# Kernel tuning notes

Hardware: AMD Instinct MI355X
Metric: run time of the kernel (lower is better)

Reference implementation:

```python
import jax, jax.numpy as jnp
import numpy as np

N, E, G = 100000, 800000, 1000
N_IN, NHID, HEADS, NOUT = 128, 32, 4, 768
HC = NHID * HEADS


def setup_inputs() -> dict:
    key = jax.random.key(0)
    ks = jax.random.split(key, 12)
    s = 1.0 / np.sqrt(N_IN)
    inp = {
        "x": jax.random.normal(ks[0], (N, N_IN), jnp.float32),
        "edge_index": jax.random.randint(ks[1], (2, E), 0, N, jnp.int64),
        "batch": jnp.sort(jax.random.randint(ks[2], (N,), 0, G, jnp.int64)),
        "Wq": jax.random.uniform(ks[3], (N_IN, HC), jnp.float32, -s, s),
        "bq": jnp.zeros((HC,), jnp.float32),
        "Wk": jax.random.uniform(ks[4], (N_IN, HC), jnp.float32, -s, s),
        "bk": jnp.zeros((HC,), jnp.float32),
        "Wv": jax.random.uniform(ks[5], (N_IN, HC), jnp.float32, -s, s),
        "bv": jnp.zeros((HC,), jnp.float32),
        "Wskip": jax.random.uniform(ks[6], (N_IN, HC), jnp.float32, -s, s),
        "bskip": jnp.zeros((HC,), jnp.float32),
        "Wbeta": jax.random.uniform(ks[7], (3 * HC, 1), jnp.float32, -1.0 / np.sqrt(3 * HC), 1.0 / np.sqrt(3 * HC)),
        "W2": jax.random.uniform(ks[8], (HC, NOUT), jnp.float32, -1.0 / np.sqrt(HC), 1.0 / np.sqrt(HC)),
        "b2": jnp.zeros((NOUT,), jnp.float32),
    }
    return inp


def _transformer_net(x, edge_index, batch, Wq, bq, Wk, bk, Wv, bv, Wskip, bskip, Wbeta, W2, b2):
    src, dst = edge_index[0], edge_index[1]  # messages src -> dst
    q = (x @ Wq + bq).reshape(N, HEADS, NHID)
    k = (x @ Wk + bk).reshape(N, HEADS, NHID)
    v = (x @ Wv + bv).reshape(N, HEADS, NHID)
    # edge-wise attention logits [E, H]
    alpha = jnp.einsum('ehc,ehc->eh', q[dst], k[src]) / np.sqrt(NHID)
    # segment softmax over incoming edges of each destination node
    m = jax.ops.segment_max(alpha, dst, num_segments=N)  # [N, H]
    e = jnp.exp(alpha - m[dst])
    denom = jax.ops.segment_sum(e, dst, num_segments=N)  # [N, H]
    attn = e / (denom[dst] + 1e-16)  # [E, H]
    msg = v[src] * attn[..., None]  # [E, H, C]
    out = jax.ops.segment_sum(msg, dst, num_segments=N).reshape(N, HC)
    # beta gating (root skip)
    skip = x @ Wskip + bskip  # [N, HC]
    beta = jax.nn.sigmoid(jnp.concatenate([out, skip, out - skip], axis=-1) @ Wbeta)  # [N, 1]
    out = beta * skip + (1.0 - beta) * out
    # LeakyReLU (default slope 0.01)
    out = jnp.where(out >= 0, out, 0.01 * out)
    # global mean pool per graph
    sums = jax.ops.segment_sum(out, batch, num_segments=G)  # [G, HC]
    cnts = jax.ops.segment_sum(jnp.ones((N,), out.dtype), batch, num_segments=G)
    pooled = sums / jnp.maximum(cnts, 1.0)[:, None]
    return pooled @ W2 + b2  # [G, NOUT]


def reference(x, edge_index, batch, Wq, bq, Wk, bk, Wv, bv, Wskip, bskip, Wbeta, W2, b2):
    return _transformer_net(x, edge_index, batch, Wq, bq, Wk, bk, Wv, bv, Wskip, bskip, Wbeta, W2, b2)
```

## Files before the change

### kernel.cpp

```cpp
#include <hip/hip_runtime.h>
#include <hip/hip_bf16.h>
#include <math.h>

#define NIN 128
#define HC 128
#define NOUT 768

typedef __attribute__((ext_vector_type(8))) short bf16x8;
typedef __attribute__((ext_vector_type(4))) float f32x4;
typedef __attribute__((ext_vector_type(4))) unsigned short ushort4v;
typedef __attribute__((ext_vector_type(8))) unsigned short ushort8v;

__device__ __forceinline__ unsigned short f2bf(float f) {
    __hip_bfloat16 h = __float2bfloat16(f);
    return *(unsigned short*)&h;
}

__device__ __forceinline__ void bf8_unpack(ushort8v u, float* f) {
    #pragma unroll
    for (int j = 0; j < 8; ++j)
        f[j] = __uint_as_float(((unsigned int)u[j]) << 16);
}

__global__ __launch_bounds__(256) void prep_w(
    const float* __restrict__ Wq, const float* __restrict__ Wk,
    const float* __restrict__ Wv, const float* __restrict__ Wsk,
    unsigned short* __restrict__ Wtb)
{
    const float* W = (blockIdx.x == 0) ? Wq : (blockIdx.x == 1) ? Wk
                   : (blockIdx.x == 2) ? Wv : Wsk;
    unsigned short* out = Wtb + (size_t)blockIdx.x * 128 * 128;
    const int t = threadIdx.x;
    for (int s = 0; s < 16; ++s) {
        const int f = t + s * 256;
        const int k = f >> 5;
        const int n = (f & 31) * 4;
        float4 w4 = *(const float4*)(W + (size_t)k * 128 + n);
        out[(size_t)(n    ) * 128 + k] = f2bf(w4.x);
        out[(size_t)(n + 1) * 128 + k] = f2bf(w4.y);
        out[(size_t)(n + 2) * 128 + k] = f2bf(w4.z);
        out[(size_t)(n + 3) * 128 + k] = f2bf(w4.w);
    }
}

__global__ __launch_bounds__(256, 4) void gemm_kv(
    const float* __restrict__ x, const unsigned short* __restrict__ Wtb,
    const float* __restrict__ bk, const float* __restrict__ bv,
    __hip_bfloat16* __restrict__ kout, __hip_bfloat16* __restrict__ vout, int N)
{
    __shared__ unsigned short At[128][136];
    const int tid = threadIdx.x;
    const int lane = tid & 63;
    const int wave = tid >> 6;
    const int rowBase = blockIdx.x * 128;
    const bool full = (rowBase + 128 <= N);

    #pragma unroll
    for (int s = 0; s < 16; ++s) {
        const int f = tid + s * 256;
        const int r = f >> 5;
        const int cl = (f & 31) * 4;
        const int gr = rowBase + r;
        float4 a4 = make_float4(0.f, 0.f, 0.f, 0.f);
        if (full || gr < N) a4 = *(const float4*)(x + (size_t)gr * 128 + cl);
        ushort4v u;
        u.x = f2bf(a4.x); u.y = f2bf(a4.y); u.z = f2bf(a4.z); u.w = f2bf(a4.w);
        *(ushort4v*)&At[r][cl] = u;
    }
    __syncthreads();

    bf16x8 afr[2][4];
    #pragma unroll
    for (int m = 0; m < 2; ++m)
        #pragma unroll
        for (int kk = 0; kk < 4; ++kk)
            afr[m][kk] = *(bf16x8*)&At[wave * 32 + m * 16 + (lane & 15)]
                                    [kk * 32 + (lane >> 4) * 8];

    const int colb = lane & 15;
    const int kofs = (lane >> 4) * 8;
    const int g4   = (lane >> 4) * 4;

    const int w2 = blockIdx.y;
    const unsigned short* Wp = Wtb + (size_t)(1 + w2) * 128 * 128;
    const float* bias = (w2 == 0) ? bk : bv;
    __hip_bfloat16* out = (w2 == 0) ? kout : vout;

    f32x4 acc[2][8];
    #pragma unroll
    for (int m = 0; m < 2; ++m)
        #pragma unroll
        for (int nr = 0; nr < 8; ++nr)
            acc[m][nr] = (f32x4){0.f, 0.f, 0.f, 0.f};

    #pragma unroll
    for (int nr = 0; nr < 8; ++nr) {
        bf16x8 bfr[4];
        #pragma unroll
        for (int kk = 0; kk < 4; ++kk)
            bfr[kk] = *(const bf16x8*)(Wp + (size_t)(nr * 16 + colb) * 128
                                           + kk * 32 + kofs);
        #pragma unroll
        for (int kk = 0; kk < 4; ++kk) {
            #pragma unroll
            for (int m = 0; m < 2; ++m)
                acc[m][nr] = __builtin_amdgcn_mfma_f32_16x16x32_bf16(
                    bfr[kk], afr[m][kk], acc[m][nr], 0, 0, 0);
        }
    }

    #pragma unroll
    for (int m = 0; m < 2; ++m) {
        const int xrow = rowBase + wave * 32 + m * 16 + (lane & 15);
        if (full || xrow < N) {
            #pragma unroll
            for (int nr = 0; nr < 8; ++nr) {
                const int colb4 = nr * 16 + g4;
                const float4 b4 = *(const float4*)(bias + colb4);
                ushort4v pk;
                pk.x = f2bf(acc[m][nr][0] + b4.x);
                pk.y = f2bf(acc[m][nr][1] + b4.y);
                pk.z = f2bf(acc[m][nr][2] + b4.z);
                pk.w = f2bf(acc[m][nr][3] + b4.w);
                *(ushort4v*)(out + (size_t)xrow * 128 + colb4) = pk;
            }
        }
    }
}

__global__ __launch_bounds__(256) void hist_kernel(
    const int* __restrict__ ei, int* __restrict__ cnt, int E)
{
    const int e = blockIdx.x * 256 + threadIdx.x;
    if (e < E) atomicAdd(cnt + ei[E + e], 1);
}

__global__ __launch_bounds__(1024) void scan_part(
    const int* __restrict__ cnt, int* __restrict__ start,
    int* __restrict__ bsum, int N)
{
    __shared__ int wsum[16];
    const int tid = threadIdx.x;
    const int lane = tid & 63;
    const int w = tid >> 6;
    const int i = blockIdx.x * 1024 + tid;
    const int v = (i < N) ? cnt[i] : 0;
    int xv = v;
    #pragma unroll
    for (int off = 1; off < 64; off <<= 1) {
        const int y = __shfl_up(xv, off, 64);
        if (lane >= off) xv += y;
    }
    if (lane == 63) wsum[w] = xv;
    __syncthreads();
    if (tid < 16) {
        int y = wsum[tid];
        #pragma unroll
        for (int off = 1; off < 16; off <<= 1) {
            const int z = __shfl_up(y, off, 64);
            if (tid >= off) y += z;
        }
        wsum[tid] = y;
    }
    __syncthreads();
    const int excl = (w > 0 ? wsum[w - 1] : 0) + xv - v;
    if (i < N) start[i] = excl;
    if (tid == 1023) bsum[blockIdx.x] = wsum[15];
}

__global__ __launch_bounds__(128) void scan_bsum(int* __restrict__ bsum, int NB)
{
    const int tid = threadIdx.x;
    __shared__ int w0tot;
    const int v = (tid < NB) ? bsum[tid] : 0;
    int xv = v;
    const int lane = tid & 63;
    #pragma unroll
    for (int off = 1; off < 64; off <<= 1) {
        const int y = __shfl_up(xv, off, 64);
        if (lane >= off) xv += y;
    }
    if (tid == 63) w0tot = xv;
    __syncthreads();
    const int incl = xv + ((tid >= 64) ? w0tot : 0);
    if (tid < NB) bsum[tid] = incl - v;
}

__global__ __launch_bounds__(256) void scan_add(
    int* __restrict__ start, int* __restrict__ cursor,
    const int* __restrict__ bsum, int N)
{
    const int i = blockIdx.x * 256 + threadIdx.x;
    if (i < N) {
        const int s = start[i] + bsum[i >> 10];
        start[i] = s;
        cursor[i] = s;
    }
}

__global__ __launch_bounds__(256) void scatter_kernel(
    const int* __restrict__ ei, int* __restrict__ cursor,
    int* __restrict__ csr_src, int E)
{
    const int e = blockIdx.x * 256 + threadIdx.x;
    if (e < E) {
        const int d = ei[E + e];
        const int pos = atomicAdd(cursor + d, 1);
        csr_src[pos] = ei[e];
    }
}

__global__ __launch_bounds__(256) void node_aggr_fused(
    const float* __restrict__ x, const unsigned short* __restrict__ Wtb,
    const float* __restrict__ bq, const float* __restrict__ bsk,
    const __hip_bfloat16* __restrict__ k, const __hip_bfloat16* __restrict__ v,
    const int* __restrict__ start, const int* __restrict__ cnt,
    const int* __restrict__ csr_src, const float* __restrict__ Wbeta,
    __hip_bfloat16* __restrict__ gout, int N)
{
    __shared__ unsigned short At[16][136];
    __shared__ float q_lds[16][132];
    __shared__ float sk_lds[16][132];

    const int tid = threadIdx.x;
    const int lane = tid & 63;
    const int wave = tid >> 6;
    const int n0 = blockIdx.x * 16;

    #pragma unroll
    for (int s = 0; s < 2; ++s) {
        const int f = tid + s * 256;
        const int r = f >> 5;
        const int cl = (f & 31) * 4;
        const int gr = n0 + r;
        float4 a4 = make_float4(0.f, 0.f, 0.f, 0.f);
        if (gr < N) a4 = *(const float4*)(x + (size_t)gr * 128 + cl);
        ushort4v u;
        u.x = f2bf(a4.x); u.y = f2bf(a4.y); u.z = f2bf(a4.z); u.w = f2bf(a4.w);
        *(ushort4v*)&At[r][cl] = u;
    }
    __syncthreads();

    {
        bf16x8 afr[4];
        #pragma unroll
        for (int kk = 0; kk < 4; ++kk)
            afr[kk] = *(bf16x8*)&At[lane & 15][kk * 32 + (lane >> 4) * 8];
        const int colb = lane & 15;
        const int kofs = (lane >> 4) * 8;
        const int g4m  = (lane >> 4) * 4;
        const int rm   = lane & 15;

        f32x4 acc[2][2];
        #pragma unroll
        for (int a = 0; a < 2; ++a)
            #pragma unroll
            for (int b = 0; b < 2; ++b)
                acc[a][b] = (f32x4){0.f, 0.f, 0.f, 0.f};

        #pragma unroll
        for (int nr2 = 0; nr2 < 2; ++nr2) {
            const int nr = wave * 2 + nr2;
            #pragma unroll
            for (int wsel = 0; wsel < 2; ++wsel) {
                const unsigned short* Wp = Wtb + (size_t)(wsel == 0 ? 0 : 3) * 128 * 128;
                bf16x8 bfr[4];
                #pragma unroll
                for (int kk = 0; kk < 4; ++kk)
                    bfr[kk] = *(const bf16x8*)(Wp + (size_t)(nr * 16 + colb) * 128
                                                   + kk * 32 + kofs);
                #pragma unroll
                for (int kk = 0; kk < 4; ++kk)
                    acc[wsel][nr2] = __builtin_amdgcn_mfma_f32_16x16x32_bf16(
                        bfr[kk], afr[kk], acc[wsel][nr2], 0, 0, 0);
            }
        }

        #pragma unroll
        for (int nr2 = 0; nr2 < 2; ++nr2) {
            const int col = (wave * 2 + nr2) * 16 + g4m;
            #pragma unroll
            for (int j = 0; j < 4; ++j) {
                q_lds[rm][col + j]  = acc[0][nr2][j] + bq[col + j];
                sk_lds[rm][col + j] = acc[1][nr2][j] + bsk[col + j];
            }
        }
    }
    __syncthreads();

    const int g  = lane >> 4;
    const int t  = lane & 15;
    const int ch = t * 8;
    const int r  = wave * 4 + g;
    const int n  = n0 + r;
    const bool nok = (n < N);
    const float scale = 0.17677669529663687f;

    float qv[8];
    {
        float4 q0 = *(float4*)&q_lds[r][ch];
        float4 q1 = *(float4*)&q_lds[r][ch + 4];
        qv[0]=q0.x; qv[1]=q0.y; qv[2]=q0.z; qv[3]=q0.w;
        qv[4]=q1.x; qv[5]=q1.y; qv[6]=q1.z; qv[7]=q1.w;
    }

    const int s0v = nok ? start[n] : 0;
    const int e1v = nok ? s0v + cnt[n] : 0;
    float den = 0.f;
    float acc[8];
    #pragma unroll
    for (int j = 0; j < 8; ++j) acc[j] = 0.f;

    for (int base = s0v; base < e1v; base += 16) {
        const int nblk = min(16, e1v - base);
        const int sidx = csr_src[base + min(t, nblk - 1)];
        int j = 0;
        for (; j + 1 < nblk; j += 2) {
            const int sa = __shfl(sidx, g * 16 + j, 64);
            const int sb = __shfl(sidx, g * 16 + j + 1, 64);
            const ushort8v k8a = *(const ushort8v*)(k + (size_t)sa * HC + ch);
            const ushort8v v8a = *(const ushort8v*)(v + (size_t)sa * HC + ch);
            const ushort8v k8b = *(const ushort8v*)(k + (size_t)sb * HC + ch);
            const ushort8v v8b = *(const ushort8v*)(v + (size_t)sb * HC + ch);
            float kfa[8], vfa[8], kfb[8], vfb[8];
            bf8_unpack(k8a, kfa); bf8_unpack(v8a, vfa);
            bf8_unpack(k8b, kfb); bf8_unpack(v8b, vfb);
            float pa = 0.f, pb = 0.f;
            #pragma unroll
            for (int jj = 0; jj < 8; ++jj) {
                pa = fmaf(kfa[jj], qv[jj], pa);
                pb = fmaf(kfb[jj], qv[jj], pb);
            }
            pa += __shfl_xor(pa, 1, 64);
            pa += __shfl_xor(pa, 2, 64);
            pb += __shfl_xor(pb, 1, 64);
            pb += __shfl_xor(pb, 2, 64);
            const float exa = __expf(pa * scale);
            const float exb = __expf(pb * scale);
            den += exa + exb;
            #pragma unroll
            for (int jj = 0; jj < 8; ++jj)
                acc[jj] = fmaf(vfa[jj], exa, fmaf(vfb[jj], exb, acc[jj]));
        }
        if (j < nblk) {
            const int sa = __shfl(sidx, g * 16 + j, 64);
            const ushort8v k8a = *(const ushort8v*)(k + (size_t)sa * HC + ch);
            const ushort8v v8a = *(const ushort8v*)(v + (size_t)sa * HC + ch);
            float kfa[8], vfa[8];
            bf8_unpack(k8a, kfa); bf8_unpack(v8a, vfa);
            float pa = 0.f;
            #pragma unroll
            for (int jj = 0; jj < 8; ++jj) pa = fmaf(kfa[jj], qv[jj], pa);
            pa += __shfl_xor(pa, 1, 64);
            pa += __shfl_xor(pa, 2, 64);
            const float exa = __expf(pa * scale);
            den += exa;
            #pragma unroll
            for (int jj = 0; jj < 8; ++jj) acc[jj] = fmaf(vfa[jj], exa, acc[jj]);
        }
    }

    const float inv = 1.f / (den + 1e-16f);
    float o[8], sk[8];
    {
        float4 s0f = *(float4*)&sk_lds[r][ch];
        float4 s1f = *(float4*)&sk_lds[r][ch + 4];
        sk[0]=s0f.x; sk[1]=s0f.y; sk[2]=s0f.z; sk[3]=s0f.w;
        sk[4]=s1f.x; sk[5]=s1f.y; sk[6]=s1f.z; sk[7]=s1f.w;
    }
    float part = 0.f;
    #pragma unroll
    for (int j = 0; j < 8; ++j) {
        o[j] = acc[j] * inv;
        part += o[j] * Wbeta[ch + j] + sk[j] * Wbeta[HC + ch + j]
              + (o[j] - sk[j]) * Wbeta[2 * HC + ch + j];
    }
    part += __shfl_xor(part, 1, 64);
    part += __shfl_xor(part, 2, 64);
    part += __shfl_xor(part, 4, 64);
    part += __shfl_xor(part, 8, 64);

    const float beta = 1.f / (1.f + __expf(-part));
    if (nok) {
        union { unsigned short h[8]; ushort8v v8; } pk;
        #pragma unroll
        for (int j = 0; j < 8; ++j) {
            float rv = beta * sk[j] + (1.f - beta) * o[j];
            rv = (rv >= 0.f) ? rv : 0.01f * rv;
            pk.h[j] = f2bf(rv);
        }
        *(ushort8v*)(gout + (size_t)n * HC + ch) = pk.v8;
    }
}

__global__ __launch_bounds__(256) void pool_final(
    const __hip_bfloat16* __restrict__ gout, const int* __restrict__ batch,
    const float* __restrict__ W2, const float* __restrict__ b2,
    float* __restrict__ out, int N, int G)
{
    const int g0 = blockIdx.x * 4;
    __shared__ float p[4][HC];
    const int wave = threadIdx.x >> 6;
    const int lane = threadIdx.x & 63;
    const int g = g0 + wave;
    if (g < G) {
        int lo = 0, hi = N;
        while (lo < hi) { const int m = (lo + hi) >> 1; if (batch[m] < g) lo = m + 1; else hi = m; }
        int lo2 = lo, hi2 = N;
        while (lo2 < hi2) { const int m = (lo2 + hi2) >> 1; if (batch[m] < g + 1) lo2 = m + 1; else hi2 = m; }
        float a0 = 0.f, a1 = 0.f;
        for (int r = lo; r < lo2; ++r) {
            const __hip_bfloat162 g2 = *(const __hip_bfloat162*)(gout + (size_t)r * HC + 2 * lane);
            a0 += __bfloat162float(g2.x);
            a1 += __bfloat162float(g2.y);
        }
        const float invc = 1.f / fmaxf((float)(lo2 - lo), 1.f);
        p[wave][2 * lane]     = a0 * invc;
        p[wave][2 * lane + 1] = a1 * invc;
    }
    __syncthreads();
    const int t = threadIdx.x;
    for (int j = t; j < NOUT; j += 256) {
        const float bj = b2[j];
        float a0 = bj, a1 = bj, a2 = bj, a3 = bj;
        #pragma unroll 4
        for (int c = 0; c < HC; ++c) {
            const float w = W2[(size_t)c * NOUT + j];
            a0 = fmaf(p[0][c], w, a0);
            a1 = fmaf(p[1][c], w, a1);
            a2 = fmaf(p[2][c], w, a2);
            a3 = fmaf(p[3][c], w, a3);
        }
        if (g0     < G) out[(size_t)(g0    ) * NOUT + j] = a0;
        if (g0 + 1 < G) out[(size_t)(g0 + 1) * NOUT + j] = a1;
        if (g0 + 2 < G) out[(size_t)(g0 + 2) * NOUT + j] = a2;
        if (g0 + 3 < G) out[(size_t)(g0 + 3) * NOUT + j] = a3;
    }
}

extern "C" void kernel_launch(void* const* d_in, const int* in_sizes, int n_in,
                              void* d_out, int out_size, void* d_ws, size_t ws_size,
                              hipStream_t stream) {
    const float* x     = (const float*)d_in[0];
    const int*   ei    = (const int*)d_in[1];
    const int*   batch = (const int*)d_in[2];
    const float* Wq  = (const float*)d_in[3];  const float* bq  = (const float*)d_in[4];
    const float* Wk  = (const float*)d_in[5];  const float* bk  = (const float*)d_in[6];
    const float* Wv  = (const float*)d_in[7];  const float* bv  = (const float*)d_in[8];
    const float* Wsk = (const float*)d_in[9];  const float* bsk = (const float*)d_in[10];
    const float* Wbeta = (const float*)d_in[11];
    const float* W2  = (const float*)d_in[12]; const float* b2  = (const float*)d_in[13];

    const int N = in_sizes[0] / NIN;
    const int E = in_sizes[1] / 2;
    const int G = out_size / NOUT;

    char* ws = (char*)d_ws;
    const size_t nbQ = (size_t)N * HC * sizeof(__hip_bfloat16);
    __hip_bfloat16* kk_  = (__hip_bfloat16*)(ws);
    __hip_bfloat16* vv   = (__hip_bfloat16*)(ws + nbQ);
    char* p0 = ws + 2 * nbQ;
    unsigned short* Wtb = (unsigned short*)p0;            p0 += 4 * 128 * 128 * sizeof(unsigned short);
    int* cnt    = (int*)p0;                               p0 += (size_t)N * sizeof(int);
    int* start  = (int*)p0;                               p0 += (size_t)N * sizeof(int);
    int* cursor = (int*)p0;                               p0 += (size_t)N * sizeof(int);
    int* bsum   = (int*)p0;                               p0 += 1024 * sizeof(int);
    int* csr    = (int*)p0;                               p0 += (size_t)E * sizeof(int);
    __hip_bfloat16* gout = (__hip_bfloat16*)p0;

    hipMemsetAsync(cnt, 0, (size_t)N * sizeof(int), stream);

    const int eb = (E + 255) / 256;
    const int NB = (N + 1023) / 1024;
    hist_kernel<<<eb, 256, 0, stream>>>(ei, cnt, E);
    scan_part<<<NB, 1024, 0, stream>>>(cnt, start, bsum, N);
    scan_bsum<<<1, 128, 0, stream>>>(bsum, NB);
    scan_add<<<(N + 255) / 256, 256, 0, stream>>>(start, cursor, bsum, N);
    scatter_kernel<<<eb, 256, 0, stream>>>(ei, cursor, csr, E);

    prep_w<<<4, 256, 0, stream>>>(Wq, Wk, Wv, Wsk, Wtb);
    dim3 gKV((N + 127) / 128, 2);
    gemm_kv<<<gKV, 256, 0, stream>>>(x, Wtb, bk, bv, kk_, vv, N);

    node_aggr_fused<<<(N + 15) / 16, 256, 0, stream>>>(x, Wtb, bq, bsk, kk_, vv,
                                                       start, cnt, csr, Wbeta,
                                                       gout, N);

    pool_final<<<(G + 3) / 4, 256, 0, stream>>>(gout, batch, W2, b2,
                                                (float*)d_out, N, G);
}
```

Measured before the change: 324.4 us.

## Interleave K and V rows into one buffer and unroll edge gather by four

Stores each node's K and V bf16 rows next to each other in a single 512-byte row, so the per-edge gather of a source node's K and V touches one contiguous region instead of two distant arrays. The edge loop in the aggregation kernel is also unrolled from two to four edges per iteration, which puts more independent gather loads in flight. The cost is higher register pressure from the extra unrolling, which may lower occupancy.

```diff
diff --git a/kernel.cpp b/kernel.cpp
--- a/kernel.cpp
+++ b/kernel.cpp
@@ -16,10 +16,8 @@
     return *(unsigned short*)&h;
 }
 
-__device__ __forceinline__ void bf8_unpack(ushort8v u, float* f) {
-    #pragma unroll
-    for (int j = 0; j < 8; ++j)
-        f[j] = __uint_as_float(((unsigned int)u[j]) << 16);
+__device__ __forceinline__ float bfe(ushort8v u, int j) {
+    return __uint_as_float(((unsigned int)u[j]) << 16);
 }
 
 __global__ __launch_bounds__(256) void prep_w(
@@ -46,7 +44,7 @@
 __global__ __launch_bounds__(256, 4) void gemm_kv(
     const float* __restrict__ x, const unsigned short* __restrict__ Wtb,
     const float* __restrict__ bk, const float* __restrict__ bv,
-    __hip_bfloat16* __restrict__ kout, __hip_bfloat16* __restrict__ vout, int N)
+    __hip_bfloat16* __restrict__ kv, int N)
 {
     __shared__ unsigned short At[128][136];
     const int tid = threadIdx.x;
@@ -84,7 +82,7 @@
     const int w2 = blockIdx.y;
     const unsigned short* Wp = Wtb + (size_t)(1 + w2) * 128 * 128;
     const float* bias = (w2 == 0) ? bk : bv;
-    __hip_bfloat16* out = (w2 == 0) ? kout : vout;
+    const int halfOfs = w2 * 128;
 
     f32x4 acc[2][8];
     #pragma unroll
@@ -122,7 +120,7 @@
                 pk.y = f2bf(acc[m][nr][1] + b4.y);
                 pk.z = f2bf(acc[m][nr][2] + b4.z);
                 pk.w = f2bf(acc[m][nr][3] + b4.w);
-                *(ushort4v*)(out + (size_t)xrow * 128 + colb4) = pk;
+                *(ushort4v*)(kv + (size_t)xrow * 256 + halfOfs + colb4) = pk;
             }
         }
     }
@@ -213,7 +211,7 @@
 __global__ __launch_bounds__(256) void node_aggr_fused(
     const float* __restrict__ x, const unsigned short* __restrict__ Wtb,
     const float* __restrict__ bq, const float* __restrict__ bsk,
-    const __hip_bfloat16* __restrict__ k, const __hip_bfloat16* __restrict__ v,
+    const __hip_bfloat16* __restrict__ kv,
     const int* __restrict__ start, const int* __restrict__ cnt,
     const int* __restrict__ csr_src, const float* __restrict__ Wbeta,
     __hip_bfloat16* __restrict__ gout, int N)
@@ -315,48 +313,56 @@
         const int nblk = min(16, e1v - base);
         const int sidx = csr_src[base + min(t, nblk - 1)];
         int j = 0;
-        for (; j + 1 < nblk; j += 2) {
-            const int sa = __shfl(sidx, g * 16 + j, 64);
+        for (; j + 3 < nblk; j += 4) {
+            const int sa = __shfl(sidx, g * 16 + j,     64);
             const int sb = __shfl(sidx, g * 16 + j + 1, 64);
-            const ushort8v k8a = *(const ushort8v*)(k + (size_t)sa * HC + ch);
-            const ushort8v v8a = *(const ushort8v*)(v + (size_t)sa * HC + ch);
-            const ushort8v k8b = *(const ushort8v*)(k + (size_t)sb * HC + ch);
-            const ushort8v v8b = *(const ushort8v*)(v + (size_t)sb * HC + ch);
-            float kfa[8], vfa[8], kfb[8], vfb[8];
-            bf8_unpack(k8a, kfa); bf8_unpack(v8a, vfa);
-            bf8_unpack(k8b, kfb); bf8_unpack(v8b, vfb);
-            float pa = 0.f, pb = 0.f;
+            const int sc = __shfl(sidx, g * 16 + j + 2, 64);
+            const int sd = __shfl(sidx, g * 16 + j + 3, 64);
+            const ushort8v k8a = *(const ushort8v*)(kv + (size_t)sa * 256 + ch);
+            const ushort8v k8b = *(const ushort8v*)(kv + (size_t)sb * 256 + ch);
+            const ushort8v k8c = *(const ushort8v*)(kv + (size_t)sc * 256 + ch);
+            const ushort8v k8d = *(const ushort8v*)(kv + (size_t)sd * 256 + ch);
+            const ushort8v v8a = *(const ushort8v*)(kv + (size_t)sa * 256 + 128 + ch);
+            const ushort8v v8b = *(const ushort8v*)(kv + (size_t)sb * 256 + 128 + ch);
+            const ushort8v v8c = *(const ushort8v*)(kv + (size_t)sc * 256 + 128 + ch);
+            const ushort8v v8d = *(const ushort8v*)(kv + (size_t)sd * 256 + 128 + ch);
+            float pa = 0.f, pb = 0.f, pc = 0.f, pd = 0.f;
             #pragma unroll
             for (int jj = 0; jj < 8; ++jj) {
-                pa = fmaf(kfa[jj], qv[jj], pa);
-                pb = fmaf(kfb[jj], qv[jj], pb);
+                pa = fmaf(bfe(k8a, jj), qv[jj], pa);
+                pb = fmaf(bfe(k8b, jj), qv[jj], pb);
+                pc = fmaf(bfe(k8c, jj), qv[jj], pc);
+                pd = fmaf(bfe(k8d, jj), qv[jj], pd);
             }
-            pa += __shfl_xor(pa, 1, 64);
-            pa += __shfl_xor(pa, 2, 64);
-            pb += __shfl_xor(pb, 1, 64);
-            pb += __shfl_xor(pb, 2, 64);
+            pa += __shfl_xor(pa, 1, 64);  pb += __shfl_xor(pb, 1, 64);
+            pc += __shfl_xor(pc, 1, 64);  pd += __shfl_xor(pd, 1, 64);
+            pa += __shfl_xor(pa, 2, 64);  pb += __shfl_xor(pb, 2, 64);
+            pc += __shfl_xor(pc, 2, 64);  pd += __shfl_xor(pd, 2, 64);
             const float exa = __expf(pa * scale);
             const float exb = __expf(pb * scale);
-            den += exa + exb;
+            const float exc = __expf(pc * scale);
+            const float exd = __expf(pd * scale);
+            den += (exa + exb) + (exc + exd);
             #pragma unroll
             for (int jj = 0; jj < 8; ++jj)
-                acc[jj] = fmaf(vfa[jj], exa, fmaf(vfb[jj], exb, acc[jj]));
-        }
-        if (j < nblk) {
+                acc[jj] = fmaf(bfe(v8a, jj), exa,
+                          fmaf(bfe(v8b, jj), exb,
+                          fmaf(bfe(v8c, jj), exc,
+                          fmaf(bfe(v8d, jj), exd, acc[jj]))));
+        }
+        for (; j < nblk; ++j) {
             const int sa = __shfl(sidx, g * 16 + j, 64);
-            const ushort8v k8a = *(const ushort8v*)(k + (size_t)sa * HC + ch);
-            const ushort8v v8a = *(const ushort8v*)(v + (size_t)sa * HC + ch);
-            float kfa[8], vfa[8];
-            bf8_unpack(k8a, kfa); bf8_unpack(v8a, vfa);
+            const ushort8v k8a = *(const ushort8v*)(kv + (size_t)sa * 256 + ch);
+            const ushort8v v8a = *(const ushort8v*)(kv + (size_t)sa * 256 + 128 + ch);
             float pa = 0.f;
             #pragma unroll
-            for (int jj = 0; jj < 8; ++jj) pa = fmaf(kfa[jj], qv[jj], pa);
+            for (int jj = 0; jj < 8; ++jj) pa = fmaf(bfe(k8a, jj), qv[jj], pa);
             pa += __shfl_xor(pa, 1, 64);
             pa += __shfl_xor(pa, 2, 64);
             const float exa = __expf(pa * scale);
             den += exa;
             #pragma unroll
-            for (int jj = 0; jj < 8; ++jj) acc[jj] = fmaf(vfa[jj], exa, acc[jj]);
+            for (int jj = 0; jj < 8; ++jj) acc[jj] = fmaf(bfe(v8a, jj), exa, acc[jj]);
         }
     }
 
@@ -457,8 +463,7 @@
 
     char* ws = (char*)d_ws;
     const size_t nbQ = (size_t)N * HC * sizeof(__hip_bfloat16);
-    __hip_bfloat16* kk_  = (__hip_bfloat16*)(ws);
-    __hip_bfloat16* vv   = (__hip_bfloat16*)(ws + nbQ);
+    __hip_bfloat16* kv = (__hip_bfloat16*)(ws);
     char* p0 = ws + 2 * nbQ;
     unsigned short* Wtb = (unsigned short*)p0;            p0 += 4 * 128 * 128 * sizeof(unsigned short);
     int* cnt    = (int*)p0;                               p0 += (size_t)N * sizeof(int);
@@ -480,9 +485,9 @@
 
     prep_w<<<4, 256, 0, stream>>>(Wq, Wk, Wv, Wsk, Wtb);
     dim3 gKV((N + 127) / 128, 2);
-    gemm_kv<<<gKV, 256, 0, stream>>>(x, Wtb, bk, bv, kk_, vv, N);
-
-    node_aggr_fused<<<(N + 15) / 16, 256, 0, stream>>>(x, Wtb, bq, bsk, kk_, vv,
+    gemm_kv<<<gKV, 256, 0, stream>>>(x, Wtb, bk, bv, kv, N);
+
+    node_aggr_fused<<<(N + 15) / 16, 256, 0, stream>>>(x, Wtb, bq, bsk, kv,
                                                        start, cnt, csr, Wbeta,
                                                        gout, N);
 
```

After: 329.7 us. No clear change (+1.6%).
